# Kernel tuning notes

Hardware: AMD Instinct MI355X
Metric: run time of the kernel (lower is better)

The kernel has to match this reference:

```python
import jax, jax.numpy as jnp
import numpy as np

# ---- static configuration (mirrors module init kwargs) ----
RADIUS = 8.0
MAX_NEIGHBORS = 32          # max_num_neighbors_threshold
MAX_REP = (2, 2, 0)         # static: rep = min(ceil(radius*inv_min_dist), threshold) = 2 for a1,a2; pbc[2]=False -> 0
B, N_ATOMS = 32, 128
CELL_EDGE = 4.0


def _unit_cells():
    # torch.cartesian_prod over arange(-rep, rep+1) per dim; pbc z disabled -> single 0
    ax = [np.arange(-r, r + 1, dtype=np.float32) for r in MAX_REP]
    g = np.stack(np.meshgrid(*ax, indexing='ij'), axis=-1).reshape(-1, 3)
    return jnp.asarray(g)  # [C, 3], C = 5*5*1 = 25


def setup_inputs() -> dict:
    key = jax.random.key(0)
    k1, k2 = jax.random.split(key)
    # near-cubic cells ~4A with small perturbation (keeps rep clamped at threshold=2)
    cell = (CELL_EDGE * jnp.eye(3, dtype=jnp.float32)[None] +
            0.05 * jax.random.normal(k2, (B, 3, 3), dtype=jnp.float32))
    # atoms at fractional coords in [0,1): pos = frac @ cell
    frac = jax.random.uniform(k1, (B, N_ATOMS, 3), dtype=jnp.float32)
    pos = jnp.einsum('bnf,bfk->bnk', frac, cell)
    return {'pos': pos, 'cell': cell}


def reference(pos, cell):
    """PBC radius-graph construction (gen_edges_from_batch), padded form.

    Candidate edges live on a fixed grid [B, i, j, c]: i = index1 (center atom),
    j = index2 (neighbor), c = periodic image. Returns:
      edge_dist       [B,N,N,C] f32  distance (0 where edge invalid)
      edge_cell_type  [B,N,N,C] i32  linearized cell-offset id (0 where invalid)
      edge_mask       [B,N,N,C] bool edge survives radius + self + kNN truncation
      num_neighbors_image [B]   i32  per-image edge counts (clamped), as in torch
    """
    u = _unit_cells()                         # [C,3]
    C = u.shape[0]
    # pbc offsets: offset_c = u_c @ cell_b  (matches cell_offsets.bmm(cell))
    off = jnp.einsum('ci,bik->bck', u, cell)  # [B,C,3]

    # distance vectors: pos[index2] - pos[index1] + offset (get_pbc_distances convention)
    dvec = (pos[:, None, :, None, :] - pos[:, :, None, None, :]
            + off[:, None, None, :, :])       # [B,N,N,C,3]
    d2 = jnp.sum(dvec * dvec, axis=-1)        # [B,N,N,C]

    within = (d2 <= RADIUS * RADIUS) & (d2 > 1e-4)

    # --- sort-based neighbor truncation per center atom i (get_max_neighbors_mask) ---
    num_atoms = B * N_ATOMS
    rows = jnp.where(within, d2, jnp.inf).reshape(num_atoms, N_ATOMS * C)
    order = jnp.argsort(rows, axis=1)         # stable: ties keep (j,c) order as torch
    ranks = jnp.argsort(order, axis=1)        # inverse permutation = rank of each cand
    keep = (ranks < MAX_NEIGHBORS).reshape(B, N_ATOMS, N_ATOMS, C) & within

    # per-image clamped neighbor counts (segment_csr of clamped segment_coo)
    num_nb = jnp.sum(within, axis=(2, 3)).astype(jnp.int32)          # [B,N]
    num_neighbors_image = jnp.sum(jnp.minimum(num_nb, MAX_NEIGHBORS), axis=1)

    safe_d2 = jnp.where(keep, d2, 1.0)
    edge_dist = jnp.where(keep, jnp.sqrt(safe_d2), 0.0)

    # linearized cell type: (offsets + max_rep) . [nr1*nr2, nr1, 1] with nr = 2*rep+1
    nr = np.array([2 * r + 1 for r in MAX_REP])
    mults = jnp.asarray([nr[1] * nr[2], nr[1], 1], dtype=jnp.int32)  # matches torch code
    ct = jnp.sum((u.astype(jnp.int32) + jnp.asarray(MAX_REP, jnp.int32)) * mults, axis=-1)  # [C]
    edge_cell_type = jnp.where(keep, ct[None, None, None, :], 0).astype(jnp.int32)

    return edge_dist, edge_cell_type, keep, num_neighbors_image
```

## Files before the change

kernel.cpp:

```cpp
#include <hip/hip_runtime.h>
#include <math.h>
#include <stdint.h>

#define NATOMS   128
#define NCELLS   25
#define NCAND    (NATOMS * NCELLS)
#define MAXNB    32
#define R2       64.0f
#define BLK      256
#define NGRP     (NCAND / 4)
#define KEYCAP   256

__global__ __launch_bounds__(BLK) void graph_kernel(
    const float* __restrict__ pos, const float* __restrict__ cell,
    float* __restrict__ out_dist, float* __restrict__ out_ctype,
    float* __restrict__ out_mask, float* __restrict__ out_nb)
{
    __shared__ float4 s_pos4[NATOMS];
    __shared__ float4 s_off4[NCELLS];
    __shared__ float  s_ct[NCELLS];
    __shared__ unsigned s_hist[256];
    __shared__ unsigned s_wtot[4];
    __shared__ int s_wred[4];
    __shared__ unsigned long long s_keys[KEYCAP];
    __shared__ unsigned s_cnt;
    __shared__ int s_binsel, s_need, s_tot, s_att;
    __shared__ unsigned long long s_K;

    const int bi   = blockIdx.x;
    const int b    = bi >> 7;
    const int i    = bi & 127;
    const int tid  = threadIdx.x;
    const int lane = tid & 63;
    const int w    = tid >> 6;

    if (tid < NATOMS) {
        const float* p = pos + (b * NATOMS + tid) * 3;
        s_pos4[tid] = make_float4(p[0], p[1], p[2], 0.0f);
    }
    if (tid >= 160 && tid < 160 + NCELLS) {
        int c = tid - 160;
        float ux = (float)(c / 5 - 2);
        float uy = (float)(c % 5 - 2);
        float ox = __fadd_rn(__fmul_rn(ux, cell[b*9+0]), __fmul_rn(uy, cell[b*9+3]));
        float oy = __fadd_rn(__fmul_rn(ux, cell[b*9+1]), __fmul_rn(uy, cell[b*9+4]));
        float oz = __fadd_rn(__fmul_rn(ux, cell[b*9+2]), __fmul_rn(uy, cell[b*9+5]));
        s_off4[c] = make_float4(ox, oy, oz, 0.0f);
        s_ct[c] = (float)(5 * (c / 5) + 5 * (c % 5));
    }
    s_hist[tid] = 0u;
    if (tid == 0) { s_cnt = 0; s_binsel = -1; s_need = 0; s_att = 0; s_K = ~0ULL; }
    __syncthreads();

    const float4 ctr = s_pos4[i];

    float d2r[16];
    int local = 0;
    #pragma unroll
    for (int k = 0; k < 4; k++) {
        int g = k * BLK + tid;
        if (g < NGRP) {
            int f0 = g * 4;
            int j = f0 / 25;
            int c = f0 - j * 25;
            #pragma unroll
            for (int e = 0; e < 4; e++) {
                float4 p = s_pos4[j];
                float4 o = s_off4[c];
                float dx = __fadd_rn(__fsub_rn(p.x, ctr.x), o.x);
                float dy = __fadd_rn(__fsub_rn(p.y, ctr.y), o.y);
                float dz = __fadd_rn(__fsub_rn(p.z, ctr.z), o.z);
                float d2 = __fadd_rn(__fadd_rn(__fmul_rn(dx,dx), __fmul_rn(dy,dy)),
                                     __fmul_rn(dz,dz));
                bool within = (d2 <= R2) && (d2 > 1e-4f);
                d2r[k*4+e] = within ? d2 : __builtin_inff();
                if (within) {
                    local++;
                    if (d2 < 16.0f)
                        atomicAdd(&s_hist[(int)(d2 * 16.0f)], 1u);
                }
                c++; if (c == 25) { c = 0; j++; }
            }
        }
    }
    for (int o = 32; o; o >>= 1) local += __shfl_down(local, o);
    if (lane == 0) s_wred[w] = local;
    __syncthreads();
    if (tid == 0) {
        int tot = s_wred[0] + s_wred[1] + s_wred[2] + s_wred[3];
        s_tot = tot;
        atomicAdd(&out_nb[b], (float)(tot < MAXNB ? tot : MAXNB));
    }
    __syncthreads();

    if (s_tot > MAXNB) {
        for (int att = 0; att < 2 && s_binsel < 0; att++) {
            if (att == 1) {
                s_hist[tid] = 0u;
                __syncthreads();
                #pragma unroll
                for (int k = 0; k < 4; k++) {
                    int g = k * BLK + tid;
                    if (g < NGRP) {
                        #pragma unroll
                        for (int e = 0; e < 4; e++) {
                            float d2 = d2r[k*4+e];
                            if (d2 < 64.5f) {
                                int bin = (int)(d2 * 4.0f);
                                if (bin > 255) bin = 255;
                                atomicAdd(&s_hist[bin], 1u);
                            }
                        }
                    }
                }
                __syncthreads();
            }
            unsigned h = s_hist[tid];
            int v = (int)h;
            #pragma unroll
            for (int off = 1; off < 64; off <<= 1) {
                int u = __shfl_up(v, off, 64);
                if (lane >= off) v += u;
            }
            if (lane == 63) s_wtot[w] = (unsigned)v;
            __syncthreads();
            unsigned pre = 0;
            for (int ww = 0; ww < w; ww++) pre += s_wtot[ww];
            unsigned htot = s_wtot[0] + s_wtot[1] + s_wtot[2] + s_wtot[3];
            unsigned ci = (unsigned)v + pre, ce = ci - h;
            if (htot >= MAXNB && h > 0 && ce < MAXNB && ci >= MAXNB) {
                s_binsel = tid;
                s_need   = MAXNB - (int)ce;
                s_att    = att;
            }
            __syncthreads();
        }

        const int   binsel = s_binsel;
        const float sc  = s_att ? 4.0f  : 16.0f;
        const float lim = s_att ? 64.5f : 16.0f;
        #pragma unroll
        for (int k = 0; k < 4; k++) {
            int g = k * BLK + tid;
            if (g < NGRP) {
                int f0 = g * 4;
                #pragma unroll
                for (int e = 0; e < 4; e++) {
                    float d2 = d2r[k*4+e];
                    if (d2 < lim) {
                        int bin = (int)(d2 * sc);
                        if (bin > 255) bin = 255;
                        if (bin == binsel) {
                            unsigned idx = atomicAdd(&s_cnt, 1u);
                            if (idx < KEYCAP)
                                s_keys[idx] =
                                    ((unsigned long long)__float_as_uint(d2) << 32)
                                    | (unsigned)(f0 + e);
                        }
                    }
                }
            }
        }
        __syncthreads();
        const int m = (int)s_cnt, need = s_need;
        if (m <= KEYCAP) {
            for (int p = tid; p < m; p += BLK) {
                unsigned long long kp = s_keys[p];
                int r = 0;
                for (int q = 0; q < m; q++) r += (s_keys[q] < kp);
                if (r == need - 1) s_K = kp;
            }
        } else {
            #pragma unroll 1
            for (int k = 0; k < 4; k++) {
                int g = k * BLK + tid;
                if (g >= NGRP) continue;
                int f0 = g * 4;
                for (int e = 0; e < 4; e++) {
                    float d2 = d2r[k*4+e];
                    if (d2 >= lim) continue;
                    int bin = (int)(d2 * sc);
                    if (bin > 255) bin = 255;
                    if (bin != binsel) continue;
                    unsigned long long kf =
                        ((unsigned long long)__float_as_uint(d2) << 32)
                        | (unsigned)(f0 + e);
                    int r = 0;
                    for (int q = 0; q < NCAND; q++) {
                        int jq = q / 25, cq = q - (q / 25) * 25;
                        float4 p = s_pos4[jq];
                        float4 o = s_off4[cq];
                        float dx = __fadd_rn(__fsub_rn(p.x, ctr.x), o.x);
                        float dy = __fadd_rn(__fsub_rn(p.y, ctr.y), o.y);
                        float dz = __fadd_rn(__fsub_rn(p.z, ctr.z), o.z);
                        float dq = __fadd_rn(__fadd_rn(__fmul_rn(dx,dx),
                                                       __fmul_rn(dy,dy)),
                                             __fmul_rn(dz,dz));
                        bool within = (dq <= R2) && (dq > 1e-4f);
                        if (!within || dq >= lim) continue;
                        int bq = (int)(dq * sc);
                        if (bq > 255) bq = 255;
                        if (bq != binsel) continue;
                        unsigned long long kq =
                            ((unsigned long long)__float_as_uint(dq) << 32)
                            | (unsigned)q;
                        r += (kq < kf);
                    }
                    if (r == need - 1) s_K = kf;
                }
            }
        }
        __syncthreads();
    }
    const unsigned long long K = s_K;

    const long long base = (long long)bi * NCAND;
    float4* o0 = (float4*)(out_dist  + base);
    float4* o1 = (float4*)(out_ctype + base);
    float4* o2 = (float4*)(out_mask  + base);
    #pragma unroll
    for (int k = 0; k < 4; k++) {
        int g = k * BLK + tid;
        if (g < NGRP) {
            int f0 = g * 4;
            int j = f0 / 25;
            int c = f0 - j * 25;
            float4 r0, r1, r2;
            #pragma unroll
            for (int e = 0; e < 4; e++) {
                float d2 = d2r[k*4+e];
                bool within = (d2 <= R2);
                unsigned long long key =
                    ((unsigned long long)__float_as_uint(d2) << 32)
                    | (unsigned)(f0 + e);
                bool keep = within && (key <= K);
                (&r0.x)[e] = keep ? sqrtf(d2) : 0.0f;
                (&r1.x)[e] = keep ? s_ct[c] : 0.0f;
                (&r2.x)[e] = keep ? 1.0f : 0.0f;
                c++; if (c == 25) c = 0;
            }
            o0[g] = r0; o1[g] = r1; o2[g] = r2;
        }
    }
}

extern "C" void kernel_launch(void* const* d_in, const int* in_sizes, int n_in,
                              void* d_out, int out_size, void* d_ws, size_t ws_size,
                              hipStream_t stream) {
    const float* pos  = (const float*)d_in[0];
    const float* cell = (const float*)d_in[1];
    float* out = (float*)d_out;
    const long long E = 32LL * NATOMS * NATOMS * NCELLS;
    float* out_dist  = out;
    float* out_ct    = out + E;
    float* out_mask  = out + 2 * E;
    float* out_nb    = out + 3 * E;

    hipMemsetAsync(out_nb, 0, 32 * sizeof(float), stream);
    hipLaunchKernelGGL(graph_kernel, dim3(32 * NATOMS), dim3(BLK), 0, stream,
                       pos, cell, out_dist, out_ct, out_mask, out_nb);
}
```

Baseline: 190.5 us.

## Split into select and write kernels, recompute distances instead of caching

Splits the single kernel into two. The first computes per-center thresholds K, recomputing distances each pass instead of holding them in registers, and stores K in workspace. The second kernel recomputes distances and writes the three dense outputs, using twice as many blocks so each covers half a row. The aim is to reduce register pressure and let more blocks run the store-heavy phase in parallel, at the cost of extra arithmetic, a second launch and a round trip through global memory.

```diff
diff --git a/kernel.cpp b/kernel.cpp
--- a/kernel.cpp
+++ b/kernel.cpp
@@ -8,17 +8,22 @@
 #define MAXNB    32
 #define R2       64.0f
 #define BLK      256
-#define NGRP     (NCAND / 4)
 #define KEYCAP   256
 
-__global__ __launch_bounds__(BLK) void graph_kernel(
+__device__ __forceinline__ float d2_exact(float4 p, float4 ctr, float4 o) {
+    float dx = __fadd_rn(__fsub_rn(p.x, ctr.x), o.x);
+    float dy = __fadd_rn(__fsub_rn(p.y, ctr.y), o.y);
+    float dz = __fadd_rn(__fsub_rn(p.z, ctr.z), o.z);
+    return __fadd_rn(__fadd_rn(__fmul_rn(dx,dx), __fmul_rn(dy,dy)),
+                     __fmul_rn(dz,dz));
+}
+
+__global__ __launch_bounds__(BLK) void select_kernel(
     const float* __restrict__ pos, const float* __restrict__ cell,
-    float* __restrict__ out_dist, float* __restrict__ out_ctype,
-    float* __restrict__ out_mask, float* __restrict__ out_nb)
+    unsigned long long* __restrict__ ws_K, float* __restrict__ out_nb)
 {
     __shared__ float4 s_pos4[NATOMS];
     __shared__ float4 s_off4[NCELLS];
-    __shared__ float  s_ct[NCELLS];
     __shared__ unsigned s_hist[256];
     __shared__ unsigned s_wtot[4];
     __shared__ int s_wred[4];
@@ -46,7 +51,6 @@
         float oy = __fadd_rn(__fmul_rn(ux, cell[b*9+1]), __fmul_rn(uy, cell[b*9+4]));
         float oz = __fadd_rn(__fmul_rn(ux, cell[b*9+2]), __fmul_rn(uy, cell[b*9+5]));
         s_off4[c] = make_float4(ox, oy, oz, 0.0f);
-        s_ct[c] = (float)(5 * (c / 5) + 5 * (c % 5));
     }
     s_hist[tid] = 0u;
     if (tid == 0) { s_cnt = 0; s_binsel = -1; s_need = 0; s_att = 0; s_K = ~0ULL; }
@@ -54,33 +58,16 @@
 
     const float4 ctr = s_pos4[i];
 
-    float d2r[16];
     int local = 0;
-    #pragma unroll
-    for (int k = 0; k < 4; k++) {
-        int g = k * BLK + tid;
-        if (g < NGRP) {
-            int f0 = g * 4;
-            int j = f0 / 25;
-            int c = f0 - j * 25;
-            #pragma unroll
-            for (int e = 0; e < 4; e++) {
-                float4 p = s_pos4[j];
-                float4 o = s_off4[c];
-                float dx = __fadd_rn(__fsub_rn(p.x, ctr.x), o.x);
-                float dy = __fadd_rn(__fsub_rn(p.y, ctr.y), o.y);
-                float dz = __fadd_rn(__fsub_rn(p.z, ctr.z), o.z);
-                float d2 = __fadd_rn(__fadd_rn(__fmul_rn(dx,dx), __fmul_rn(dy,dy)),
-                                     __fmul_rn(dz,dz));
-                bool within = (d2 <= R2) && (d2 > 1e-4f);
-                d2r[k*4+e] = within ? d2 : __builtin_inff();
-                if (within) {
-                    local++;
-                    if (d2 < 16.0f)
-                        atomicAdd(&s_hist[(int)(d2 * 16.0f)], 1u);
-                }
-                c++; if (c == 25) { c = 0; j++; }
-            }
+    for (int g = tid; g < NCAND; g += BLK) {
+        int c = g >> 7;
+        int j = g & 127;
+        float d2 = d2_exact(s_pos4[j], ctr, s_off4[c]);
+        bool within = (d2 <= R2) && (d2 > 1e-4f);
+        if (within) {
+            local++;
+            if (d2 < 16.0f)
+                atomicAdd(&s_hist[(int)(d2 * 16.0f)], 1u);
         }
     }
     for (int o = 32; o; o >>= 1) local += __shfl_down(local, o);
@@ -98,19 +85,13 @@
             if (att == 1) {
                 s_hist[tid] = 0u;
                 __syncthreads();
-                #pragma unroll
-                for (int k = 0; k < 4; k++) {
-                    int g = k * BLK + tid;
-                    if (g < NGRP) {
-                        #pragma unroll
-                        for (int e = 0; e < 4; e++) {
-                            float d2 = d2r[k*4+e];
-                            if (d2 < 64.5f) {
-                                int bin = (int)(d2 * 4.0f);
-                                if (bin > 255) bin = 255;
-                                atomicAdd(&s_hist[bin], 1u);
-                            }
-                        }
+                for (int g = tid; g < NCAND; g += BLK) {
+                    int c = g >> 7, j = g & 127;
+                    float d2 = d2_exact(s_pos4[j], ctr, s_off4[c]);
+                    if ((d2 <= R2) && (d2 > 1e-4f)) {
+                        int bin = (int)(d2 * 4.0f);
+                        if (bin > 255) bin = 255;
+                        atomicAdd(&s_hist[bin], 1u);
                     }
                 }
                 __syncthreads();
@@ -139,25 +120,19 @@
         const int   binsel = s_binsel;
         const float sc  = s_att ? 4.0f  : 16.0f;
         const float lim = s_att ? 64.5f : 16.0f;
-        #pragma unroll
-        for (int k = 0; k < 4; k++) {
-            int g = k * BLK + tid;
-            if (g < NGRP) {
-                int f0 = g * 4;
-                #pragma unroll
-                for (int e = 0; e < 4; e++) {
-                    float d2 = d2r[k*4+e];
-                    if (d2 < lim) {
-                        int bin = (int)(d2 * sc);
-                        if (bin > 255) bin = 255;
-                        if (bin == binsel) {
-                            unsigned idx = atomicAdd(&s_cnt, 1u);
-                            if (idx < KEYCAP)
-                                s_keys[idx] =
-                                    ((unsigned long long)__float_as_uint(d2) << 32)
-                                    | (unsigned)(f0 + e);
-                        }
-                    }
+        for (int g = tid; g < NCAND; g += BLK) {
+            int c = g >> 7, j = g & 127;
+            float d2 = d2_exact(s_pos4[j], ctr, s_off4[c]);
+            bool within = (d2 <= R2) && (d2 > 1e-4f);
+            if (within && d2 < lim) {
+                int bin = (int)(d2 * sc);
+                if (bin > 255) bin = 255;
+                if (bin == binsel) {
+                    unsigned idx = atomicAdd(&s_cnt, 1u);
+                    if (idx < KEYCAP)
+                        s_keys[idx] =
+                            ((unsigned long long)__float_as_uint(d2) << 32)
+                            | (unsigned)(j * NCELLS + c);
                 }
             }
         }
@@ -171,76 +146,100 @@
                 if (r == need - 1) s_K = kp;
             }
         } else {
-            #pragma unroll 1
-            for (int k = 0; k < 4; k++) {
-                int g = k * BLK + tid;
-                if (g >= NGRP) continue;
-                int f0 = g * 4;
-                for (int e = 0; e < 4; e++) {
-                    float d2 = d2r[k*4+e];
-                    if (d2 >= lim) continue;
-                    int bin = (int)(d2 * sc);
-                    if (bin > 255) bin = 255;
-                    if (bin != binsel) continue;
-                    unsigned long long kf =
-                        ((unsigned long long)__float_as_uint(d2) << 32)
-                        | (unsigned)(f0 + e);
-                    int r = 0;
-                    for (int q = 0; q < NCAND; q++) {
-                        int jq = q / 25, cq = q - (q / 25) * 25;
-                        float4 p = s_pos4[jq];
-                        float4 o = s_off4[cq];
-                        float dx = __fadd_rn(__fsub_rn(p.x, ctr.x), o.x);
-                        float dy = __fadd_rn(__fsub_rn(p.y, ctr.y), o.y);
-                        float dz = __fadd_rn(__fsub_rn(p.z, ctr.z), o.z);
-                        float dq = __fadd_rn(__fadd_rn(__fmul_rn(dx,dx),
-                                                       __fmul_rn(dy,dy)),
-                                             __fmul_rn(dz,dz));
-                        bool within = (dq <= R2) && (dq > 1e-4f);
-                        if (!within || dq >= lim) continue;
-                        int bq = (int)(dq * sc);
-                        if (bq > 255) bq = 255;
-                        if (bq != binsel) continue;
-                        unsigned long long kq =
-                            ((unsigned long long)__float_as_uint(dq) << 32)
-                            | (unsigned)q;
-                        r += (kq < kf);
-                    }
-                    if (r == need - 1) s_K = kf;
+            for (int g = tid; g < NCAND; g += BLK) {
+                int c = g >> 7, j = g & 127;
+                float d2 = d2_exact(s_pos4[j], ctr, s_off4[c]);
+                bool within = (d2 <= R2) && (d2 > 1e-4f);
+                if (!within || d2 >= lim) continue;
+                int bin = (int)(d2 * sc);
+                if (bin > 255) bin = 255;
+                if (bin != binsel) continue;
+                unsigned long long kf =
+                    ((unsigned long long)__float_as_uint(d2) << 32)
+                    | (unsigned)(j * NCELLS + c);
+                int r = 0;
+                for (int q = 0; q < NCAND; q++) {
+                    int cq = q >> 7, jq = q & 127;
+                    float dq = d2_exact(s_pos4[jq], ctr, s_off4[cq]);
+                    bool wq = (dq <= R2) && (dq > 1e-4f);
+                    if (!wq || dq >= lim) continue;
+                    int bq = (int)(dq * sc);
+                    if (bq > 255) bq = 255;
+                    if (bq != binsel) continue;
+                    unsigned long long kq =
+                        ((unsigned long long)__float_as_uint(dq) << 32)
+                        | (unsigned)(jq * NCELLS + cq);
+                    r += (kq < kf);
                 }
+                if (r == need - 1) s_K = kf;
             }
         }
         __syncthreads();
     }
-    const unsigned long long K = s_K;
-
-    const long long base = (long long)bi * NCAND;
-    float4* o0 = (float4*)(out_dist  + base);
-    float4* o1 = (float4*)(out_ctype + base);
-    float4* o2 = (float4*)(out_mask  + base);
-    #pragma unroll
-    for (int k = 0; k < 4; k++) {
-        int g = k * BLK + tid;
-        if (g < NGRP) {
-            int f0 = g * 4;
-            int j = f0 / 25;
-            int c = f0 - j * 25;
-            float4 r0, r1, r2;
-            #pragma unroll
-            for (int e = 0; e < 4; e++) {
-                float d2 = d2r[k*4+e];
-                bool within = (d2 <= R2);
-                unsigned long long key =
-                    ((unsigned long long)__float_as_uint(d2) << 32)
-                    | (unsigned)(f0 + e);
-                bool keep = within && (key <= K);
-                (&r0.x)[e] = keep ? sqrtf(d2) : 0.0f;
-                (&r1.x)[e] = keep ? s_ct[c] : 0.0f;
-                (&r2.x)[e] = keep ? 1.0f : 0.0f;
-                c++; if (c == 25) c = 0;
-            }
-            o0[g] = r0; o1[g] = r1; o2[g] = r2;
-        }
+    if (tid == 0) ws_K[bi] = s_K;
+}
+
+__global__ __launch_bounds__(BLK) void write_kernel(
+    const float* __restrict__ pos, const float* __restrict__ cell,
+    const unsigned long long* __restrict__ ws_K,
+    float* __restrict__ out_dist, float* __restrict__ out_ctype,
+    float* __restrict__ out_mask)
+{
+    __shared__ float4 s_pos4[NATOMS];
+    __shared__ float4 s_off4[NCELLS];
+    __shared__ float  s_ct[NCELLS];
+
+    const int bx   = blockIdx.x;
+    const int bi   = bx >> 1;
+    const int half = bx & 1;
+    const int b    = bi >> 7;
+    const int i    = bi & 127;
+    const int tid  = threadIdx.x;
+
+    if (tid < NATOMS) {
+        const float* p = pos + (b * NATOMS + tid) * 3;
+        s_pos4[tid] = make_float4(p[0], p[1], p[2], 0.0f);
+    }
+    if (tid >= 160 && tid < 160 + NCELLS) {
+        int c = tid - 160;
+        float ux = (float)(c / 5 - 2);
+        float uy = (float)(c % 5 - 2);
+        float ox = __fadd_rn(__fmul_rn(ux, cell[b*9+0]), __fmul_rn(uy, cell[b*9+3]));
+        float oy = __fadd_rn(__fmul_rn(ux, cell[b*9+1]), __fmul_rn(uy, cell[b*9+4]));
+        float oz = __fadd_rn(__fmul_rn(ux, cell[b*9+2]), __fmul_rn(uy, cell[b*9+5]));
+        s_off4[c] = make_float4(ox, oy, oz, 0.0f);
+        s_ct[c] = (float)(5 * (c / 5) + 5 * (c % 5));
+    }
+    __syncthreads();
+
+    const unsigned long long K = ws_K[bi];
+    const float4 ctr = s_pos4[i];
+
+    const long long gbase = (long long)bi * (NCAND / 4) + half * 400;
+    float4* o0 = (float4*)out_dist  + gbase;
+    float4* o1 = (float4*)out_ctype + gbase;
+    float4* o2 = (float4*)out_mask  + gbase;
+
+    for (int g = tid; g < 400; g += BLK) {
+        int f0 = g * 4;
+        int j  = (half << 6) + f0 / 25;
+        int c  = f0 - (f0 / 25) * 25;
+        int fa = half * 1600 + f0;
+        float4 r0, r1, r2;
+        #pragma unroll
+        for (int e = 0; e < 4; e++) {
+            float d2 = d2_exact(s_pos4[j], ctr, s_off4[c]);
+            bool within = (d2 <= R2) && (d2 > 1e-4f);
+            unsigned long long key =
+                ((unsigned long long)__float_as_uint(d2) << 32)
+                | (unsigned)(fa + e);
+            bool keep = within && (key <= K);
+            (&r0.x)[e] = keep ? sqrtf(d2) : 0.0f;
+            (&r1.x)[e] = keep ? s_ct[c] : 0.0f;
+            (&r2.x)[e] = keep ? 1.0f : 0.0f;
+            c++; if (c == NCELLS) { c = 0; j++; }
+        }
+        o0[g] = r0; o1[g] = r1; o2[g] = r2;
     }
 }
 
@@ -255,8 +254,11 @@
     float* out_ct    = out + E;
     float* out_mask  = out + 2 * E;
     float* out_nb    = out + 3 * E;
+    unsigned long long* ws_K = (unsigned long long*)d_ws;
 
     hipMemsetAsync(out_nb, 0, 32 * sizeof(float), stream);
-    hipLaunchKernelGGL(graph_kernel, dim3(32 * NATOMS), dim3(BLK), 0, stream,
-                       pos, cell, out_dist, out_ct, out_mask, out_nb);
-}
+    hipLaunchKernelGGL(select_kernel, dim3(32 * NATOMS), dim3(BLK), 0, stream,
+                       pos, cell, ws_K, out_nb);
+    hipLaunchKernelGGL(write_kernel, dim3(32 * NATOMS * 2), dim3(BLK), 0, stream,
+                       pos, cell, ws_K, out_dist, out_ct, out_mask);
+}
```

After: 209.3 us. 1.1x slower.
